# Kernel optimization log

Hardware: AMD Instinct MI355X
Metric: run time of the kernel (lower is better)

Reference implementation:

```python
import jax, jax.numpy as jnp
import numpy as np

N_HEAD = 16
D_MODEL = 1024
D_K = D_MODEL // N_HEAD  # 64
LN_EPS = 1e-5


def setup_inputs() -> dict:
    key = jax.random.key(0)
    ks = jax.random.split(key, 12)
    B, L, D = 4, 2048, D_MODEL
    std_qkv = float(np.sqrt(2.0 / (D + D_K)))
    q = jax.random.normal(ks[0], (B, L, D), jnp.float32)
    k = jax.random.normal(ks[1], (B, L, D), jnp.float32)
    v = jax.random.normal(ks[2], (B, L, D), jnp.float32)
    Wq = jax.random.normal(ks[3], (D, D), jnp.float32) * std_qkv
    Wk = jax.random.normal(ks[4], (D, D), jnp.float32) * std_qkv
    Wv = jax.random.normal(ks[5], (D, D), jnp.float32) * std_qkv
    bq = jnp.zeros((D,), jnp.float32)
    bk = jnp.zeros((D,), jnp.float32)
    bv = jnp.zeros((D,), jnp.float32)
    # xavier normal for fc: std = sqrt(2/(fan_in+fan_out))
    Wo = jax.random.normal(ks[6], (D, D), jnp.float32) * float(np.sqrt(2.0 / (D + D)))
    bo = jnp.zeros((D,), jnp.float32)
    gamma = jnp.ones((D,), jnp.float32)
    beta = jnp.zeros((D,), jnp.float32)
    return {"q": q, "k": k, "v": v, "Wq": Wq, "bq": bq, "Wk": Wk, "bk": bk,
            "Wv": Wv, "bv": bv, "Wo": Wo, "bo": bo, "gamma": gamma, "beta": beta}


def _layer_norm(x, gamma, beta):
    mu = jnp.mean(x, axis=-1, keepdims=True)
    var = jnp.mean(jnp.square(x - mu), axis=-1, keepdims=True)
    return (x - mu) * jax.lax.rsqrt(var + LN_EPS) * gamma + beta


def reference(q, k, v, Wq, bq, Wk, bk, Wv, bv, Wo, bo, gamma, beta):
    B, Lq, D = q.shape
    Lk = k.shape[1]
    h, dk = N_HEAD, D_K
    residual = q
    # projections (torch Linear: x @ W.T + b), split heads -> (h, b, l, dk)
    qh = (q @ Wq.T + bq).reshape(B, Lq, h, dk).transpose(2, 0, 1, 3)
    kh = (k @ Wk.T + bk).reshape(B, Lk, h, dk).transpose(2, 0, 1, 3)
    vh = (v @ Wv.T + bv).reshape(B, Lk, h, dk).transpose(2, 0, 1, 3)
    temp = jnp.asarray(np.power(dk, 0.5), qh.dtype)
    scores = jnp.einsum('hbqd,hbkd->hbqk', qh, kh) / temp
    attn = jax.nn.softmax(scores, axis=-1)  # softmax over key dim (dim=2 of bmm view)
    out = jnp.einsum('hbqk,hbkd->hbqd', attn, vh)
    # (h,b,lq,dk) -> (b,lq,h*dk)
    out = out.transpose(1, 2, 0, 3).reshape(B, Lq, D)
    out = out @ Wo.T + bo  # dropout p=0.0 -> identity
    out = _layer_norm(out + residual, gamma, beta)
    attn_flat = attn.reshape(h * B, Lq, Lk)  # matches torch (n_head*sz_b, lq, lk)
    return out, attn_flat
```

## Files before the change

kernel.cpp:

```cpp
#include <hip/hip_runtime.h>
#include <stdint.h>

typedef short bf16x8 __attribute__((ext_vector_type(8)));
typedef float f32x4 __attribute__((ext_vector_type(4)));
typedef unsigned short us4 __attribute__((ext_vector_type(4)));
typedef unsigned short us8 __attribute__((ext_vector_type(8)));
typedef unsigned uint2v __attribute__((ext_vector_type(2)));
typedef unsigned u32x4 __attribute__((ext_vector_type(4)));

#define SCL 0.18033688011112042f

__device__ __forceinline__ unsigned short f2bf(float f) {
  union { float f; unsigned u; } v; v.f = f;
  unsigned r = v.u + 0x7fffu + ((v.u >> 16) & 1u);
  return (unsigned short)(r >> 16);
}

__device__ __forceinline__ unsigned cvtpk(float lo, float hi) {
  unsigned r;
  asm("v_cvt_pk_bf16_f32 %0, %1, %2" : "=v"(r) : "v"(lo), "v"(hi));
  return r;
}

__device__ __forceinline__ float bf2f(unsigned short h) {
  union { unsigned u; float f; } v; v.u = ((unsigned)h) << 16; return v.f;
}

#define GL2LDS(g, l) __builtin_amdgcn_global_load_lds( \
    (const __attribute__((address_space(1))) void*)(g), \
    (__attribute__((address_space(3))) void*)(l), 16, 0, 0)

__global__ __launch_bounds__(256) void convert_all(
    const float* __restrict__ q, const float* __restrict__ k, const float* __restrict__ v,
    const float* __restrict__ wq, const float* __restrict__ wk, const float* __restrict__ wv,
    const float* __restrict__ wo,
    unsigned short* __restrict__ qb, unsigned short* __restrict__ kb, unsigned short* __restrict__ vb,
    unsigned short* __restrict__ wqb, unsigned short* __restrict__ wkb, unsigned short* __restrict__ wvb,
    unsigned short* __restrict__ wob)
{
  const long NB = 8388608, NW = 1048576;
  long i = ((long)blockIdx.x * 256 + threadIdx.x) * 4;
  if (i >= 3*NB + 4*NW) return;
  const float* src; unsigned short* dst; long off;
  if (i < NB)              { src = q;  dst = qb;  off = i; }
  else if (i < 2*NB)       { src = k;  dst = kb;  off = i - NB; }
  else if (i < 3*NB)       { src = v;  dst = vb;  off = i - 2*NB; }
  else if (i < 3*NB+NW)    { src = wq; dst = wqb; off = i - 3*NB; }
  else if (i < 3*NB+2*NW)  { src = wk; dst = wkb; off = i - 3*NB - NW; }
  else if (i < 3*NB+3*NW)  { src = wv; dst = wvb; off = i - 3*NB - 2*NW; }
  else                     { src = wo; dst = wob; off = i - 3*NB - 3*NW; }
  float4 x = *(const float4*)(src + off);
  us4 o; o.x = f2bf(x.x); o.y = f2bf(x.y); o.z = f2bf(x.z); o.w = f2bf(x.w);
  *(us4*)(dst + off) = o;
}

__global__ __launch_bounds__(256, 2) void qkv_gemm(
    const unsigned short* __restrict__ qb, const unsigned short* __restrict__ kb,
    const unsigned short* __restrict__ vb,
    const unsigned short* __restrict__ wqb, const unsigned short* __restrict__ wkb,
    const unsigned short* __restrict__ wvb,
    const float* __restrict__ bq, const float* __restrict__ bk, const float* __restrict__ bv,
    unsigned short* __restrict__ qh, unsigned short* __restrict__ kh,
    unsigned short* __restrict__ vt)
{
  const int flat = blockIdx.x + (blockIdx.y << 6);
  const int xcd = flat & 7, ii = flat >> 3;
  const int m0 = (xcd * 8 + (ii & 7)) * 128;
  const int n0 = (ii >> 3) * 128;

  const int tid = threadIdx.x, lane = tid & 63, w = tid >> 6;
  const int wr = w >> 1, wc = w & 1;
  const int lg = lane >> 4, ll = lane & 15;

  __shared__ __align__(16) char smem_q[32768];
  unsigned short* As = (unsigned short*)smem_q;
  unsigned short* Bs = (unsigned short*)(smem_q + 16384);
  unsigned short* T  = (unsigned short*)smem_q;

  const unsigned short* Xs_[3] = {qb, kb, vb};
  const unsigned short* Ws_[3] = {wqb, wkb, wvb};
  const float* bias_[3] = {bq, bk, bv};

#define STAGE_G(buf) do { \
    char* lA_ = (char*)As + (buf)*8192 + w*2048; \
    char* lB_ = (char*)Bs + (buf)*8192 + w*2048; \
    GL2LDS(gA, lA_); GL2LDS(gA + 32768, lA_ + 1024); \
    GL2LDS(gB, lB_); GL2LDS(gB + 32768, lB_ + 1024); \
    gA += 64; gB += 64; } while (0)

  for (int z = 0; z < 3; ++z) {
    const unsigned short* X = Xs_[z];
    const unsigned short* W = Ws_[z];
    const float* bias = bias_[z];
    unsigned short* dqh = (z == 0) ? qh : kh;
    const float sc = (z == 0) ? SCL : 1.0f;

    f32x4 acc[4][4] = {};

    const char* gA = (const char*)X + ((size_t)(m0 + w*32 + (lane >> 2)) * 1024) * 2 + (lane & 3) * 16;
    const char* gB = (const char*)W + ((size_t)(n0 + w*32 + (lane >> 2)) * 1024) * 2 + (lane & 3) * 16;

    STAGE_G(0);
    __syncthreads();

    for (int k0 = 0; k0 < 1024; k0 += 32) {
      const int cur = (k0 >> 5) & 1;
      if (k0 < 992) STAGE_G(cur ^ 1);
      const unsigned short* Ac = As + cur * 4096;
      const unsigned short* Bc = Bs + cur * 4096;
      bf16x8 xa[4], wb[4];
      const int kc = lg * 8;
#pragma unroll
      for (int f = 0; f < 4; ++f) xa[f] = *(const bf16x8*)&Ac[(wr*64 + f*16 + ll)*32 + kc];
#pragma unroll
      for (int f = 0; f < 4; ++f) wb[f] = *(const bf16x8*)&Bc[(wc*64 + f*16 + ll)*32 + kc];
      if (z < 2) {
#pragma unroll
        for (int fn = 0; fn < 4; ++fn)
#pragma unroll
          for (int fm = 0; fm < 4; ++fm)
            acc[fn][fm] = __builtin_amdgcn_mfma_f32_16x16x32_bf16(wb[fn], xa[fm], acc[fn][fm], 0, 0, 0);
      } else {
#pragma unroll
        for (int fm = 0; fm < 4; ++fm)
#pragma unroll
          for (int fn = 0; fn < 4; ++fn)
            acc[fm][fn] = __builtin_amdgcn_mfma_f32_16x16x32_bf16(xa[fm], wb[fn], acc[fm][fn], 0, 0, 0);
      }
      __syncthreads();
    }

    const int b_ = m0 >> 11;
    if (z < 2) {
#pragma unroll
      for (int half = 0; half < 2; ++half) {
        __syncthreads();
        if (wr == half) {
#pragma unroll
          for (int fn = 0; fn < 4; ++fn) {
            const int n_l = wc*64 + fn*16 + lg*4;
            const float4 b4 = *(const float4*)&bias[n0 + n_l];
#pragma unroll
            for (int fm = 0; fm < 4; ++fm) {
              us4 pk;
              pk.x = f2bf((acc[fn][fm][0] + b4.x) * sc);
              pk.y = f2bf((acc[fn][fm][1] + b4.y) * sc);
              pk.z = f2bf((acc[fn][fm][2] + b4.z) * sc);
              pk.w = f2bf((acc[fn][fm][3] + b4.w) * sc);
              *(us4*)&T[(fm*16 + ll)*130 + n_l] = pk;
            }
          }
        }
        __syncthreads();
        const int seg = tid >> 3, off = (tid & 7) * 8;
#pragma unroll
        for (int it = 0; it < 4; ++it) {
          const int s = it*32 + seg;
          const int ml = s >> 1, nh = (s & 1) << 6;
          us8 v = *(const us8*)&T[ml*130 + nh + off];
          const int m_g = m0 + half*64 + ml;
          const int l_ = m_g & 2047;
          const int h = (n0 + nh) >> 6;
          *(us8*)&dqh[((size_t)(h*4 + b_)*2048 + l_)*64 + off] = v;
        }
      }
    } else {
#pragma unroll
      for (int half = 0; half < 2; ++half) {
        __syncthreads();
        if (wc == half) {
#pragma unroll
          for (int fn = 0; fn < 4; ++fn) {
            const float bias_n = bias[n0 + half*64 + fn*16 + ll];
#pragma unroll
            for (int fm = 0; fm < 4; ++fm) {
              us4 pk;
              pk.x = f2bf(acc[fm][fn][0] + bias_n);
              pk.y = f2bf(acc[fm][fn][1] + bias_n);
              pk.z = f2bf(acc[fm][fn][2] + bias_n);
              pk.w = f2bf(acc[fm][fn][3] + bias_n);
              *(us4*)&T[(fn*16 + ll)*130 + wr*64 + fm*16 + lg*4] = pk;
            }
          }
        }
        __syncthreads();
        const int row = tid >> 4, mc = (tid & 15) * 8;
#pragma unroll
        for (int it = 0; it < 4; ++it) {
          const int rr = it*16 + row;
          us8 v = *(const us8*)&T[rr*130 + mc];
          const int n_g = n0 + half*64 + rr;
          const int h = n_g >> 6, dkk = n_g & 63;
          const int l_ = (m0 + mc) & 2047;
          *(us8*)&vt[((size_t)(h*4 + b_)*64 + dkk)*2048 + l_] = v;
        }
      }
    }
    __syncthreads();
  }
}

__global__ __launch_bounds__(256, 2) void attn_kernel(
    const unsigned short* __restrict__ qh, const unsigned short* __restrict__ kh,
    const unsigned short* __restrict__ vt, float* __restrict__ probs,
    unsigned short* __restrict__ attn_o)
{
  const int bid = blockIdx.x;
  const int xcd = bid & 7;
  const int idx = bid >> 3;
  const int hb  = xcd * 8 + (idx & 7);
  const int qt  = idx >> 3;

  const int tid = threadIdx.x, lane = tid & 63, w = tid >> 6;
  const int wr = w >> 1, wc = w & 1;
  const int lg = lane >> 4, ll = lane & 15;

  __shared__ __align__(16) char smem[38400];
  unsigned short* Pb = (unsigned short*)smem;
  float* rs   = (float*)(smem + 36864);
  float* invl = (float*)(smem + 37888);
  float* OredP = (float*)smem;

  const size_t slab = (size_t)hb << 17;

  bf16x8 qf[4][2];
#pragma unroll
  for (int fq = 0; fq < 4; ++fq)
#pragma unroll
    for (int dh = 0; dh < 2; ++dh)
      qf[fq][dh] = *(const bf16x8*)&qh[slab + (size_t)(qt*128 + wr*64 + fq*16 + ll)*64 + dh*32 + lg*8];

  const unsigned short* Kf = kh + slab + (size_t)(wc*32 + ll)*64 + lg*8;
  const unsigned short* Vf = vt + slab + (size_t)ll*2048 + wc*32 + lg*8;

  float rsum[4] = {0.f, 0.f, 0.f, 0.f};
  for (int kt = 0; kt < 32; ++kt) {
    bf16x8 ka[2][2];
#pragma unroll
    for (int fk = 0; fk < 2; ++fk)
#pragma unroll
      for (int dh = 0; dh < 2; ++dh)
        ka[fk][dh] = *(const bf16x8*)(Kf + kt*4096 + fk*1024 + dh*32);
    f32x4 s[2][4] = {};
    __builtin_amdgcn_s_setprio(1);
#pragma unroll
    for (int dh = 0; dh < 2; ++dh)
#pragma unroll
      for (int fk = 0; fk < 2; ++fk)
#pragma unroll
        for (int fq = 0; fq < 4; ++fq)
          s[fk][fq] = __builtin_amdgcn_mfma_f32_16x16x32_bf16(ka[fk][dh], qf[fq][dh], s[fk][fq], 0, 0, 0);
    __builtin_amdgcn_s_setprio(0);
#pragma unroll
    for (int fk = 0; fk < 2; ++fk)
#pragma unroll
      for (int fq = 0; fq < 4; ++fq)
#pragma unroll
        for (int r = 0; r < 4; ++r)
          rsum[fq] += exp2f(s[fk][fq][r]);
  }

#pragma unroll
  for (int fq = 0; fq < 4; ++fq) {
    float t = rsum[fq];
    t += __shfl_xor(t, 16);
    t += __shfl_xor(t, 32);
    rsum[fq] = t;
  }
  if (lg == 0) {
#pragma unroll
    for (int fq = 0; fq < 4; ++fq)
      rs[wc*128 + wr*64 + fq*16 + ll] = rsum[fq];
  }
  __syncthreads();
  if (tid < 128) invl[tid] = 1.0f / (rs[tid] + rs[128 + tid]);
  __syncthreads();
  float inv_r[4];
#pragma unroll
  for (int fq = 0; fq < 4; ++fq) inv_r[fq] = invl[wr*64 + fq*16 + ll];

  f32x4 o[4][4] = {};
  float* pb2 = probs + ((size_t)hb << 22) + (size_t)(qt*128) * 2048;
  const int prow = tid >> 4, pcol = (tid & 15) * 4;

  auto body = [&](bf16x8 (&ka)[2][2], bf16x8 (&kan)[2][2], int kt) {
    unsigned short* Pc = Pb + (kt & 1) * 9216;
    bf16x8 vb[4];
#pragma unroll
    for (int f = 0; f < 4; ++f)
      vb[f] = *(const bf16x8*)(Vf + f*32768 + kt*64);

    f32x4 s[2][4] = {};
    __builtin_amdgcn_s_setprio(1);
#pragma unroll
    for (int dh = 0; dh < 2; ++dh)
#pragma unroll
      for (int fk = 0; fk < 2; ++fk)
#pragma unroll
        for (int fq = 0; fq < 4; ++fq)
          s[fk][fq] = __builtin_amdgcn_mfma_f32_16x16x32_bf16(ka[fk][dh], qf[fq][dh], s[fk][fq], 0, 0, 0);
    __builtin_amdgcn_s_setprio(0);

    if (kt + 1 < 32) {
#pragma unroll
      for (int fk = 0; fk < 2; ++fk)
#pragma unroll
        for (int dh = 0; dh < 2; ++dh)
          kan[fk][dh] = *(const bf16x8*)(Kf + (kt+1)*4096 + fk*1024 + dh*32);
    }

#pragma unroll
    for (int fk = 0; fk < 2; ++fk)
#pragma unroll
      for (int fq = 0; fq < 4; ++fq) {
        float p0 = exp2f(s[fk][fq][0]) * inv_r[fq];
        float p1 = exp2f(s[fk][fq][1]) * inv_r[fq];
        float p2 = exp2f(s[fk][fq][2]) * inv_r[fq];
        float p3 = exp2f(s[fk][fq][3]) * inv_r[fq];
        uint2v u; u.x = cvtpk(p0, p1); u.y = cvtpk(p2, p3);
        *(uint2v*)&Pc[(wr*64 + fq*16 + ll)*72 + wc*32 + fk*16 + lg*4] = u;
      }

    bf16x8 pa[4];
#pragma unroll
    for (int fm = 0; fm < 4; ++fm)
      pa[fm] = *(const bf16x8*)&Pc[(wr*64 + fm*16 + ll)*72 + wc*32 + lg*8];
    __builtin_amdgcn_s_setprio(1);
#pragma unroll
    for (int fm = 0; fm < 4; ++fm)
#pragma unroll
      for (int fd = 0; fd < 4; ++fd)
        o[fm][fd] = __builtin_amdgcn_mfma_f32_16x16x32_bf16(pa[fm], vb[fd], o[fm][fd], 0, 0, 0);
    __builtin_amdgcn_s_setprio(0);

    __syncthreads();

    float* pdst = pb2 + kt*64;
#pragma unroll
    for (int j = 0; j < 8; ++j) {
      const int row = j*16 + prow;
      us4 pv = *(const us4*)&Pc[row*72 + pcol];
      f32x4 pf; pf[0] = bf2f(pv.x); pf[1] = bf2f(pv.y); pf[2] = bf2f(pv.z); pf[3] = bf2f(pv.w);
      __builtin_nontemporal_store(pf, (f32x4*)(pdst + (size_t)row*2048 + pcol));
    }
  };

  bf16x8 kaA[2][2], kaB[2][2];
#pragma unroll
  for (int fk = 0; fk < 2; ++fk)
#pragma unroll
    for (int dh = 0; dh < 2; ++dh)
      kaA[fk][dh] = *(const bf16x8*)(Kf + fk*1024 + dh*32);
  for (int kt = 0; kt < 32; kt += 2) {
    body(kaA, kaB, kt);
    body(kaB, kaA, kt + 1);
  }

  __syncthreads();
  if (wc == 1) {
#pragma unroll
    for (int fm = 0; fm < 4; ++fm)
#pragma unroll
      for (int fd = 0; fd < 4; ++fd)
#pragma unroll
        for (int r = 0; r < 4; ++r)
          OredP[wr*4224 + (fm*16 + lg*4 + r)*66 + fd*16 + ll] = o[fm][fd][r];
  }
  __syncthreads();
  if (wc == 0) {
#pragma unroll
    for (int fm = 0; fm < 4; ++fm)
#pragma unroll
      for (int fd = 0; fd < 4; ++fd)
#pragma unroll
        for (int r = 0; r < 4; ++r) {
          const int ix = wr*4224 + (fm*16 + lg*4 + r)*66 + fd*16 + ll;
          OredP[ix] += o[fm][fd][r];
        }
  }
  __syncthreads();
  {
    const int b_ = hb & 3, h = hb >> 2;
    const int r_ = tid >> 1, d0 = (tid & 1) * 32;
    const float* srcp = &OredP[(r_ >> 6)*4224 + (r_ & 63)*66 + d0];
    const int mg = b_*2048 + qt*128 + r_;
    unsigned short* dst = attn_o + (size_t)mg*1024 + h*64 + d0;
#pragma unroll
    for (int g = 0; g < 4; ++g) {
      u32x4 q4;
      q4[0] = cvtpk(srcp[g*8+0], srcp[g*8+1]);
      q4[1] = cvtpk(srcp[g*8+2], srcp[g*8+3]);
      q4[2] = cvtpk(srcp[g*8+4], srcp[g*8+5]);
      q4[3] = cvtpk(srcp[g*8+6], srcp[g*8+7]);
      *(u32x4*)(dst + g*8) = q4;
    }
  }
}

__global__ __launch_bounds__(256, 2) void outproj_gemm(
    const unsigned short* __restrict__ Ain, const unsigned short* __restrict__ Wob,
    const float* __restrict__ bo, const float* __restrict__ qres, float* __restrict__ preLN)
{
  const int flat = blockIdx.x + (blockIdx.y << 6);
  const int xcd = flat & 7, ii = flat >> 3;
  const int m0 = (xcd * 8 + (ii & 7)) * 128;
  const int n0 = (ii >> 3) * 128;

  const int tid = threadIdx.x, lane = tid & 63, w = tid >> 6;
  const int wr = w >> 1, wc = w & 1;
  const int lg = lane >> 4, ll = lane & 15;

  __shared__ __align__(16) char smem_o[33792];
  unsigned short* As = (unsigned short*)smem_o;
  unsigned short* Bs = (unsigned short*)(smem_o + 16384);
  float* Tf = (float*)smem_o;

  f32x4 acc[4][4] = {};

  const char* gA = (const char*)Ain + ((size_t)(m0 + w*32 + (lane >> 2)) * 1024) * 2 + (lane & 3) * 16;
  const char* gB = (const char*)Wob + ((size_t)(n0 + w*32 + (lane >> 2)) * 1024) * 2 + (lane & 3) * 16;

  STAGE_G(0);
  __syncthreads();

  for (int k0 = 0; k0 < 1024; k0 += 32) {
    const int cur = (k0 >> 5) & 1;
    if (k0 < 992) STAGE_G(cur ^ 1);
    const unsigned short* Ac = As + cur * 4096;
    const unsigned short* Bc = Bs + cur * 4096;
    bf16x8 xa[4], wb[4];
    const int kc = lg * 8;
#pragma unroll
    for (int f = 0; f < 4; ++f) xa[f] = *(const bf16x8*)&Ac[(wr*64 + f*16 + ll)*32 + kc];
#pragma unroll
    for (int f = 0; f < 4; ++f) wb[f] = *(const bf16x8*)&Bc[(wc*64 + f*16 + ll)*32 + kc];
#pragma unroll
    for (int fn = 0; fn < 4; ++fn)
#pragma unroll
      for (int fm = 0; fm < 4; ++fm)
        acc[fn][fm] = __builtin_amdgcn_mfma_f32_16x16x32_bf16(wb[fn], xa[fm], acc[fn][fm], 0, 0, 0);
    __syncthreads();
  }

#pragma unroll
  for (int half = 0; half < 2; ++half) {
    __syncthreads();
    if (wr == half) {
#pragma unroll
      for (int fn = 0; fn < 4; ++fn) {
        const int n_l = wc*64 + fn*16 + lg*4;
        const float4 b4 = *(const float4*)&bo[n0 + n_l];
#pragma unroll
        for (int fm = 0; fm < 4; ++fm) {
          f32x4 y;
          y[0] = acc[fn][fm][0] + b4.x;
          y[1] = acc[fn][fm][1] + b4.y;
          y[2] = acc[fn][fm][2] + b4.z;
          y[3] = acc[fn][fm][3] + b4.w;
          *(f32x4*)&Tf[(fm*16 + ll)*132 + n_l] = y;
        }
      }
    }
    __syncthreads();
    const int r_ = tid >> 5, c_ = (tid & 31) * 4;
#pragma unroll
    for (int it = 0; it < 8; ++it) {
      const int ml = it*8 + r_;
      f32x4 v = *(const f32x4*)&Tf[ml*132 + c_];
      const size_t idxp = (size_t)(m0 + half*64 + ml)*1024 + n0 + c_;
      const float4 r4 = *(const float4*)&qres[idxp];
      v[0] += r4.x; v[1] += r4.y; v[2] += r4.z; v[3] += r4.w;
      *(f32x4*)&preLN[idxp] = v;
    }
  }
}

__global__ __launch_bounds__(256) void ln_kernel(
    const float* __restrict__ x, const float* __restrict__ gamma,
    const float* __restrict__ beta, float* __restrict__ out)
{
  const int row = blockIdx.x, tid = threadIdx.x;
  const float4 xv = ((const float4*)(x + (size_t)row * 1024))[tid];
  float s = xv.x + xv.y + xv.z + xv.w;
  float ss = xv.x*xv.x + xv.y*xv.y + xv.z*xv.z + xv.w*xv.w;
#pragma unroll
  for (int m = 1; m < 64; m <<= 1) { s += __shfl_xor(s, m); ss += __shfl_xor(ss, m); }
  __shared__ float red[8];
  if ((tid & 63) == 0) { red[(tid >> 6)*2] = s; red[(tid >> 6)*2 + 1] = ss; }
  __syncthreads();
  s  = red[0] + red[2] + red[4] + red[6];
  ss = red[1] + red[3] + red[5] + red[7];
  const float mu = s * (1.0f/1024.0f);
  const float var = ss * (1.0f/1024.0f) - mu*mu;
  const float rstd = rsqrtf(var + 1e-5f);
  const float4 g  = ((const float4*)gamma)[tid];
  const float4 be = ((const float4*)beta)[tid];
  float4 y;
  y.x = (xv.x - mu)*rstd*g.x + be.x;
  y.y = (xv.y - mu)*rstd*g.y + be.y;
  y.z = (xv.z - mu)*rstd*g.z + be.z;
  y.w = (xv.w - mu)*rstd*g.w + be.w;
  ((float4*)(out + (size_t)row * 1024))[tid] = y;
}

extern "C" void kernel_launch(void* const* d_in, const int* in_sizes, int n_in,
                              void* d_out, int out_size, void* d_ws, size_t ws_size,
                              hipStream_t stream) {
  const float* q     = (const float*)d_in[0];
  const float* k     = (const float*)d_in[1];
  const float* v     = (const float*)d_in[2];
  const float* Wq    = (const float*)d_in[3];
  const float* bq    = (const float*)d_in[4];
  const float* Wk    = (const float*)d_in[5];
  const float* bk    = (const float*)d_in[6];
  const float* Wv    = (const float*)d_in[7];
  const float* bv    = (const float*)d_in[8];
  const float* Wo    = (const float*)d_in[9];
  const float* bo    = (const float*)d_in[10];
  const float* gamma = (const float*)d_in[11];
  const float* beta  = (const float*)d_in[12];

  float* out   = (float*)d_out;
  float* probs = out + 8388608;

  char* ws = (char*)d_ws;
  unsigned short* qb  = (unsigned short*)(ws);
  unsigned short* kb  = (unsigned short*)(ws + 16777216);
  unsigned short* vb  = (unsigned short*)(ws + 33554432);
  unsigned short* wqb = (unsigned short*)(ws + 50331648);
  unsigned short* wkb = (unsigned short*)(ws + 52428800);
  unsigned short* wvb = (unsigned short*)(ws + 54525952);
  unsigned short* wob = (unsigned short*)(ws + 56623104);
  unsigned short* qh  = (unsigned short*)(ws + 58720256);
  unsigned short* kh  = (unsigned short*)(ws + 75497472);
  unsigned short* vt  = (unsigned short*)(ws + 92274688);
  float* preLN = (float*)(ws);
  unsigned short* attn_o = vb;

  convert_all<<<28672, 256, 0, stream>>>(q, k, v, Wq, Wk, Wv, Wo,
                                         qb, kb, vb, wqb, wkb, wvb, wob);

  dim3 g1(64, 8);
  qkv_gemm<<<g1, 256, 0, stream>>>(qb, kb, vb, wqb, wkb, wvb, bq, bk, bv, qh, kh, vt);

  attn_kernel<<<1024, 256, 0, stream>>>(qh, kh, vt, probs, attn_o);

  dim3 g3(64, 8);
  outproj_gemm<<<g3, 256, 0, stream>>>(attn_o, wob, bo, q, preLN);

  ln_kernel<<<8192, 256, 0, stream>>>(preLN, gamma, beta, out);
}
```

Measured before the change: 437.0 us.

## Fuse fp32-to-bf16 activation conversion into QKV GEMM A-tile loading

```diff
diff --git a/kernel.cpp b/kernel.cpp
--- a/kernel.cpp
+++ b/kernel.cpp
@@ -30,33 +30,27 @@
     (const __attribute__((address_space(1))) void*)(g), \
     (__attribute__((address_space(3))) void*)(l), 16, 0, 0)
 
-__global__ __launch_bounds__(256) void convert_all(
-    const float* __restrict__ q, const float* __restrict__ k, const float* __restrict__ v,
+__global__ __launch_bounds__(256) void convert_w(
     const float* __restrict__ wq, const float* __restrict__ wk, const float* __restrict__ wv,
     const float* __restrict__ wo,
-    unsigned short* __restrict__ qb, unsigned short* __restrict__ kb, unsigned short* __restrict__ vb,
-    unsigned short* __restrict__ wqb, unsigned short* __restrict__ wkb, unsigned short* __restrict__ wvb,
-    unsigned short* __restrict__ wob)
+    unsigned short* __restrict__ wqb, unsigned short* __restrict__ wkb,
+    unsigned short* __restrict__ wvb, unsigned short* __restrict__ wob)
 {
-  const long NB = 8388608, NW = 1048576;
+  const long NW = 1048576;
   long i = ((long)blockIdx.x * 256 + threadIdx.x) * 4;
-  if (i >= 3*NB + 4*NW) return;
+  if (i >= 4*NW) return;
   const float* src; unsigned short* dst; long off;
-  if (i < NB)              { src = q;  dst = qb;  off = i; }
-  else if (i < 2*NB)       { src = k;  dst = kb;  off = i - NB; }
-  else if (i < 3*NB)       { src = v;  dst = vb;  off = i - 2*NB; }
-  else if (i < 3*NB+NW)    { src = wq; dst = wqb; off = i - 3*NB; }
-  else if (i < 3*NB+2*NW)  { src = wk; dst = wkb; off = i - 3*NB - NW; }
-  else if (i < 3*NB+3*NW)  { src = wv; dst = wvb; off = i - 3*NB - 2*NW; }
-  else                     { src = wo; dst = wob; off = i - 3*NB - 3*NW; }
+  if (i < NW)        { src = wq; dst = wqb; off = i; }
+  else if (i < 2*NW) { src = wk; dst = wkb; off = i - NW; }
+  else if (i < 3*NW) { src = wv; dst = wvb; off = i - 2*NW; }
+  else               { src = wo; dst = wob; off = i - 3*NW; }
   float4 x = *(const float4*)(src + off);
   us4 o; o.x = f2bf(x.x); o.y = f2bf(x.y); o.z = f2bf(x.z); o.w = f2bf(x.w);
   *(us4*)(dst + off) = o;
 }
 
 __global__ __launch_bounds__(256, 2) void qkv_gemm(
-    const unsigned short* __restrict__ qb, const unsigned short* __restrict__ kb,
-    const unsigned short* __restrict__ vb,
+    const float* __restrict__ qf_, const float* __restrict__ kf_, const float* __restrict__ vf_,
     const unsigned short* __restrict__ wqb, const unsigned short* __restrict__ wkb,
     const unsigned short* __restrict__ wvb,
     const float* __restrict__ bq, const float* __restrict__ bk, const float* __restrict__ bv,
@@ -77,35 +71,50 @@
   unsigned short* Bs = (unsigned short*)(smem_q + 16384);
   unsigned short* T  = (unsigned short*)smem_q;
 
-  const unsigned short* Xs_[3] = {qb, kb, vb};
+  const float* Xf_[3] = {qf_, kf_, vf_};
   const unsigned short* Ws_[3] = {wqb, wkb, wvb};
   const float* bias_[3] = {bq, bk, bv};
 
-#define STAGE_G(buf) do { \
-    char* lA_ = (char*)As + (buf)*8192 + w*2048; \
+#define LOAD_A(kc0) do { \
+    a0 = *(const float4*)(gAf + (kc0)); \
+    a1 = *(const float4*)(gAf + (kc0) + 4); \
+    a2 = *(const float4*)(gAf + (kc0) + 16384); \
+    a3 = *(const float4*)(gAf + (kc0) + 16388); } while (0)
+#define WRITE_A(buf) do { \
+    u32x4 pk0, pk1; \
+    pk0[0] = cvtpk(a0.x, a0.y); pk0[1] = cvtpk(a0.z, a0.w); \
+    pk0[2] = cvtpk(a1.x, a1.y); pk0[3] = cvtpk(a1.z, a1.w); \
+    pk1[0] = cvtpk(a2.x, a2.y); pk1[1] = cvtpk(a2.z, a2.w); \
+    pk1[2] = cvtpk(a3.x, a3.y); pk1[3] = cvtpk(a3.z, a3.w); \
+    *(u32x4*)(lA0 + (buf)*4096) = pk0; \
+    *(u32x4*)(lA0 + (buf)*4096 + 512) = pk1; } while (0)
+#define STAGE_B(buf) do { \
     char* lB_ = (char*)Bs + (buf)*8192 + w*2048; \
-    GL2LDS(gA, lA_); GL2LDS(gA + 32768, lA_ + 1024); \
     GL2LDS(gB, lB_); GL2LDS(gB + 32768, lB_ + 1024); \
-    gA += 64; gB += 64; } while (0)
+    gB += 64; } while (0)
 
   for (int z = 0; z < 3; ++z) {
-    const unsigned short* X = Xs_[z];
+    const float* X = Xf_[z];
     const unsigned short* W = Ws_[z];
     const float* bias = bias_[z];
     unsigned short* dqh = (z == 0) ? qh : kh;
     const float sc = (z == 0) ? SCL : 1.0f;
 
     f32x4 acc[4][4] = {};
-
-    const char* gA = (const char*)X + ((size_t)(m0 + w*32 + (lane >> 2)) * 1024) * 2 + (lane & 3) * 16;
+    float4 a0, a1, a2, a3;
+
+    const float* gAf = X + (size_t)(m0 + w*32 + (lane >> 2)) * 1024 + (lane & 3) * 8;
+    unsigned short* lA0 = As + (size_t)(w*32 + (lane >> 2)) * 32 + (lane & 3) * 8;
     const char* gB = (const char*)W + ((size_t)(n0 + w*32 + (lane >> 2)) * 1024) * 2 + (lane & 3) * 16;
 
-    STAGE_G(0);
+    LOAD_A(0);
+    STAGE_B(0);
+    WRITE_A(0);
     __syncthreads();
 
     for (int k0 = 0; k0 < 1024; k0 += 32) {
       const int cur = (k0 >> 5) & 1;
-      if (k0 < 992) STAGE_G(cur ^ 1);
+      if (k0 < 992) { LOAD_A(k0 + 32); STAGE_B(cur ^ 1); }
       const unsigned short* Ac = As + cur * 4096;
       const unsigned short* Bc = Bs + cur * 4096;
       bf16x8 xa[4], wb[4];
@@ -127,6 +136,7 @@
           for (int fn = 0; fn < 4; ++fn)
             acc[fm][fn] = __builtin_amdgcn_mfma_f32_16x16x32_bf16(xa[fm], wb[fn], acc[fm][fn], 0, 0, 0);
       }
+      if (k0 < 992) WRITE_A(cur ^ 1);
       __syncthreads();
     }
 
@@ -396,6 +406,13 @@
     }
   }
 }
+
+#define STAGE_G(buf) do { \
+    char* lA_ = (char*)As + (buf)*8192 + w*2048; \
+    char* lB_ = (char*)Bs + (buf)*8192 + w*2048; \
+    GL2LDS(gA, lA_); GL2LDS(gA + 32768, lA_ + 1024); \
+    GL2LDS(gB, lB_); GL2LDS(gB + 32768, lB_ + 1024); \
+    gA += 64; gB += 64; } while (0)
 
 __global__ __launch_bounds__(256, 2) void outproj_gemm(
     const unsigned short* __restrict__ Ain, const unsigned short* __restrict__ Wob,
@@ -524,9 +541,6 @@
   float* probs = out + 8388608;
 
   char* ws = (char*)d_ws;
-  unsigned short* qb  = (unsigned short*)(ws);
-  unsigned short* kb  = (unsigned short*)(ws + 16777216);
-  unsigned short* vb  = (unsigned short*)(ws + 33554432);
   unsigned short* wqb = (unsigned short*)(ws + 50331648);
   unsigned short* wkb = (unsigned short*)(ws + 52428800);
   unsigned short* wvb = (unsigned short*)(ws + 54525952);
@@ -535,13 +549,12 @@
   unsigned short* kh  = (unsigned short*)(ws + 75497472);
   unsigned short* vt  = (unsigned short*)(ws + 92274688);
   float* preLN = (float*)(ws);
-  unsigned short* attn_o = vb;
-
-  convert_all<<<28672, 256, 0, stream>>>(q, k, v, Wq, Wk, Wv, Wo,
-                                         qb, kb, vb, wqb, wkb, wvb, wob);
+  unsigned short* attn_o = (unsigned short*)(ws + 33554432);
+
+  convert_w<<<4096, 256, 0, stream>>>(Wq, Wk, Wv, Wo, wqb, wkb, wvb, wob);
 
   dim3 g1(64, 8);
-  qkv_gemm<<<g1, 256, 0, stream>>>(qb, kb, vb, wqb, wkb, wvb, bq, bk, bv, qh, kh, vt);
+  qkv_gemm<<<g1, 256, 0, stream>>>(q, k, v, wqb, wkb, wvb, bq, bk, bv, qh, kh, vt);
 
   attn_kernel<<<1024, 256, 0, stream>>>(qh, kh, vt, probs, attn_o);
 
```

Result: no change. 438.2 us (+0.3%).
